# Kernel optimization log

Measured on AMD Instinct MI355X. Metric: run time of the kernel, lower is better.

The kernel has to match this reference:

```python
import jax, jax.numpy as jnp
import numpy as np

SHRINK_THRES = 0.0025
EPS = 1e-12  # F.normalize default eps


def _l2norm(v, axis=-1):
    return v / jnp.maximum(jnp.linalg.norm(v, axis=axis, keepdims=True), EPS)


def setup_inputs() -> dict:
    key = jax.random.key(0)
    ks = jax.random.split(key, 5)
    N, C, H, W = 16, 256, 64, 64
    mem_dim = 512
    x = jax.random.normal(ks[0], (N, C, H, W), dtype=jnp.float32)
    memory = jax.random.normal(ks[1], (mem_dim, C), dtype=jnp.float32) * 0.1
    memory = _l2norm(memory, axis=1)
    w1 = jax.random.normal(ks[2], (C, C // 2), dtype=jnp.float32) * (1.0 / np.sqrt(C))
    b1 = jnp.zeros((C // 2,), dtype=jnp.float32)
    w2 = jax.random.normal(ks[3], (C // 2, C), dtype=jnp.float32) * (1.0 / np.sqrt(C // 2))
    b2 = jnp.zeros((C,), dtype=jnp.float32)
    return {"x": x, "memory": memory, "w1": w1, "b1": b1, "w2": w2, "b2": b2}


def reference(x, memory, w1, b1, w2, b2):
    N, C, H, W = x.shape
    # [N,C,H,W] -> [N*H*W, C]
    x_flat = jnp.transpose(x, (0, 2, 3, 1)).reshape(-1, C)
    x_norm = _l2norm(x_flat, axis=1)
    # shared MLP over memory slots: Linear -> ReLU -> Linear -> ReLU
    m = jax.nn.relu(memory @ w1 + b1)
    m = jax.nn.relu(m @ w2 + b2)
    mem_norm = _l2norm(m, axis=1)  # [M, C]
    # cosine similarity + softmax over memory slots
    att = jax.nn.softmax(x_norm @ mem_norm.T, axis=1)  # [N*H*W, M]
    # hard shrink + L1 renormalization
    att = jax.nn.relu(att - SHRINK_THRES)
    att = att / jnp.maximum(jnp.sum(att, axis=1, keepdims=True), EPS)
    out_flat = att @ mem_norm  # [N*H*W, C]
    output = jnp.transpose(out_flat.reshape(N, H, W, C), (0, 3, 1, 2))
    att_map = jnp.transpose(att.reshape(N, H, W, -1), (0, 3, 1, 2))
    return output, att_map
```

## Files before the change

kernel.cpp:

```cpp
#include <hip/hip_runtime.h>

typedef _Float16 half8 __attribute__((ext_vector_type(8)));
typedef _Float16 half4v __attribute__((ext_vector_type(4)));
typedef float floatx4 __attribute__((ext_vector_type(4)));

#define C_DIM 256
#define M_DIM 512
#define HW 4096
#define TAU 0.0025f
#define LCAP 16

#define BAR_LGKM()                                          \
  do {                                                      \
    asm volatile("s_waitcnt lgkmcnt(0)" ::: "memory");      \
    __builtin_amdgcn_s_barrier();                           \
    __builtin_amdgcn_sched_barrier(0);                      \
  } while (0)

__global__ __launch_bounds__(256) void zero_kernel(float* __restrict__ base)
{
  const floatx4 z = {0.f, 0.f, 0.f, 0.f};
  floatx4* p = (floatx4*)base + (size_t)blockIdx.x * 256 + threadIdx.x;
#pragma unroll
  for (int k = 0; k < 16; ++k)
    __builtin_nontemporal_store(z, p + (size_t)k * 786432);
}

__global__ __launch_bounds__(128) void prep_kernel(
    const float* __restrict__ memory, const float* __restrict__ w1,
    const float* __restrict__ b1, const float* __restrict__ w2,
    const float* __restrict__ b2,
    _Float16* __restrict__ mN, float* __restrict__ mN32)
{
  __shared__ float sm[256];
  __shared__ float sh[128];
  __shared__ float s_part[2];
  __shared__ float s_tot;
  const int r = blockIdx.x;
  const int t = threadIdx.x;

  sm[t]       = memory[r * C_DIM + t];
  sm[t + 128] = memory[r * C_DIM + t + 128];
  __syncthreads();
  float acc = b1[t];
#pragma unroll 8
  for (int c = 0; c < 256; ++c) acc = fmaf(sm[c], w1[c * 128 + t], acc);
  sh[t] = fmaxf(acc, 0.f);
  __syncthreads();
  float o0 = b2[t], o1 = b2[t + 128];
#pragma unroll 8
  for (int k = 0; k < 128; ++k) {
    float h = sh[k];
    o0 = fmaf(h, w2[k * 256 + t], o0);
    o1 = fmaf(h, w2[k * 256 + t + 128], o1);
  }
  o0 = fmaxf(o0, 0.f);
  o1 = fmaxf(o1, 0.f);
  float ss = o0 * o0 + o1 * o1;
#pragma unroll
  for (int off = 32; off >= 1; off >>= 1) ss += __shfl_down(ss, off);
  if ((t & 63) == 0) s_part[t >> 6] = ss;
  __syncthreads();
  if (t == 0) s_tot = s_part[0] + s_part[1];
  __syncthreads();
  const float inv = 1.f / fmaxf(sqrtf(s_tot), 1e-12f);
  const float v0 = o0 * inv, v1 = o1 * inv;
  mN[r * C_DIM + t]        = (_Float16)v0;
  mN[r * C_DIM + t + 128]  = (_Float16)v1;
  mN32[r * C_DIM + t]       = v0;
  mN32[r * C_DIM + t + 128] = v1;
}

#define MFMA16(a, b, c) __builtin_amdgcn_mfma_f32_16x16x32_f16(a, b, c, 0, 0, 0)

__global__ __launch_bounds__(512, 6) void main_kernel(
    const float* __restrict__ x,
    const _Float16* __restrict__ mN,
    const float* __restrict__ mN32,
    float* __restrict__ out, float* __restrict__ attmap)
{
  __shared__ _Float16       Xh[32][264];
  __shared__ unsigned short s_lslot[32][LCAP];
  __shared__ float          s_lval[32][LCAP];
  __shared__ int      s_cnt[32];
  __shared__ float    s_sumsq[32];
  __shared__ float    s_sum1[32];
  __shared__ float    s_sum2[32];

  const int tid  = threadIdx.x;
  const int wave = tid >> 6;
  const int lane = tid & 63;
  const int q    = lane >> 4;
  const int c16  = lane & 15;
  const int g    = tid >> 3;
  const int pxq  = tid & 7;

  const int blk = blockIdx.x;
  const int img = blk >> 7;
  const int hw0 = (blk & 127) * 32;
  const float* __restrict__ xb = x + (size_t)img * C_DIM * HW + hw0;

  if (tid < 32) {
    s_sumsq[tid] = 0.f; s_sum1[tid] = 0.f; s_sum2[tid] = 0.f; s_cnt[tid] = 0;
  }
  __syncthreads();

  {
    floatx4 v[4];
#pragma unroll
    for (int i = 0; i < 4; ++i)
      v[i] = *(const floatx4*)(xb + (size_t)(4 * g + i) * HW + pxq * 4);
    float ps[4];
#pragma unroll
    for (int j = 0; j < 4; ++j) {
      const int p = pxq * 4 + j;
      half4v hv = {(_Float16)v[0][j], (_Float16)v[1][j], (_Float16)v[2][j], (_Float16)v[3][j]};
      *(half4v*)&Xh[p][4 * g] = hv;
      ps[j] = v[0][j] * v[0][j] + v[1][j] * v[1][j] + v[2][j] * v[2][j] + v[3][j] * v[3][j];
    }
#pragma unroll
    for (int off = 8; off < 64; off <<= 1)
#pragma unroll
      for (int j = 0; j < 4; ++j) ps[j] += __shfl_xor(ps[j], off);
    if ((lane >> 3) == 0) {
#pragma unroll
      for (int j = 0; j < 4; ++j) atomicAdd(&s_sumsq[4 * (lane & 7) + j], ps[j]);
    }
  }

  const _Float16* bp[4];
#pragma unroll
  for (int nt = 0; nt < 4; ++nt)
    bp[nt] = mN + (size_t)(wave * 64 + nt * 16 + c16) * C_DIM + q * 8;

  __syncthreads();

  floatx4 acc[2][4];
#pragma unroll
  for (int mt = 0; mt < 2; ++mt)
#pragma unroll
    for (int nt = 0; nt < 4; ++nt) {
      floatx4 z = {0.f, 0.f, 0.f, 0.f};
      acc[mt][nt] = z;
    }
#pragma unroll
  for (int kb = 0; kb < 8; ++kb) {
    half8 bv[4];
#pragma unroll
    for (int nt = 0; nt < 4; ++nt) bv[nt] = *(const half8*)(bp[nt] + kb * 32);
    const int k0 = kb * 32 + q * 8;
    half8 a0 = *(const half8*)&Xh[c16][k0];
    half8 a1 = *(const half8*)&Xh[16 + c16][k0];
#pragma unroll
    for (int nt = 0; nt < 4; ++nt) {
      acc[0][nt] = MFMA16(a0, bv[nt], acc[0][nt]);
      acc[1][nt] = MFMA16(a1, bv[nt], acc[1][nt]);
    }
  }

#pragma unroll
  for (int mt = 0; mt < 2; ++mt)
#pragma unroll
    for (int r = 0; r < 4; ++r) {
      const int m = mt * 16 + q * 4 + r;
      const float iv = 1.f / fmaxf(sqrtf(s_sumsq[m]), 1e-12f);
      float s = 0.f;
#pragma unroll
      for (int nt = 0; nt < 4; ++nt) {
        const float e = __expf(acc[mt][nt][r] * iv);
        acc[mt][nt][r] = e;
        s += e;
      }
      s += __shfl_xor(s, 1);
      s += __shfl_xor(s, 2);
      s += __shfl_xor(s, 4);
      s += __shfl_xor(s, 8);
      if (c16 == 0) atomicAdd(&s_sum1[m], s);
    }
  __syncthreads();

#pragma unroll
  for (int mt = 0; mt < 2; ++mt)
#pragma unroll
    for (int r = 0; r < 4; ++r) {
      const int m = mt * 16 + q * 4 + r;
      const float isum = 1.f / s_sum1[m];
      float s = 0.f;
#pragma unroll
      for (int nt = 0; nt < 4; ++nt) {
        const float tv = fmaxf(acc[mt][nt][r] * isum - TAU, 0.f);
        acc[mt][nt][r] = tv;
        s += tv;
      }
      s += __shfl_xor(s, 1);
      s += __shfl_xor(s, 2);
      s += __shfl_xor(s, 4);
      s += __shfl_xor(s, 8);
      if (c16 == 0) atomicAdd(&s_sum2[m], s);
    }
  __syncthreads();

#pragma unroll
  for (int mt = 0; mt < 2; ++mt) {
    float rs[4];
#pragma unroll
    for (int r = 0; r < 4; ++r)
      rs[r] = 1.f / fmaxf(s_sum2[mt * 16 + q * 4 + r], 1e-12f);
#pragma unroll
    for (int nt = 0; nt < 4; ++nt) {
      floatx4 a4 = acc[mt][nt];
      const unsigned n = wave * 64 + nt * 16 + c16;
#pragma unroll
      for (int r = 0; r < 4; ++r) {
        a4[r] *= rs[r];
        if (a4[r] > 0.f) {
          const int m = mt * 16 + q * 4 + r;
          const int idx = atomicAdd(&s_cnt[m], 1);
          if (idx < LCAP) {
            s_lslot[m][idx] = (unsigned short)n;
            s_lval[m][idx]  = a4[r];
          }
          attmap[((size_t)img * M_DIM + n) * HW + hw0 + m] = a4[r];
        }
      }
    }
  }
  BAR_LGKM();

  const int px4 = (tid & 7) * 4;
  const int chg = tid >> 3;
  int cn[4];
  int any = 0;
#pragma unroll
  for (int p = 0; p < 4; ++p) { cn[p] = min(s_cnt[px4 + p], LCAP); any += cn[p]; }
  if (any) {
    floatx4 f[4] = {{0.f,0.f,0.f,0.f},{0.f,0.f,0.f,0.f},{0.f,0.f,0.f,0.f},{0.f,0.f,0.f,0.f}};
#pragma unroll
    for (int p = 0; p < 4; ++p) {
      for (int j = 0; j < cn[p]; ++j) {
        const int slot  = s_lslot[px4 + p][j];
        const float v   = s_lval[px4 + p][j];
        const floatx4 r0 = *(const floatx4*)(mN32 + (size_t)slot * C_DIM + chg * 4);
        f[0][p] += v * r0[0]; f[1][p] += v * r0[1];
        f[2][p] += v * r0[2]; f[3][p] += v * r0[3];
      }
    }
#pragma unroll
    for (int c = 0; c < 4; ++c)
      *(floatx4*)(out + ((size_t)img * C_DIM + chg * 4 + c) * HW + hw0 + px4) = f[c];
  }
}

extern "C" void kernel_launch(void* const* d_in, const int* in_sizes, int n_in,
                              void* d_out, int out_size, void* d_ws, size_t ws_size,
                              hipStream_t stream) {
  (void)in_sizes; (void)n_in; (void)out_size; (void)ws_size;
  const float* x      = (const float*)d_in[0];
  const float* memory = (const float*)d_in[1];
  const float* w1     = (const float*)d_in[2];
  const float* b1     = (const float*)d_in[3];
  const float* w2     = (const float*)d_in[4];
  const float* b2     = (const float*)d_in[5];
  float* out    = (float*)d_out;
  float* attmap = out + (size_t)16 * C_DIM * HW;

  _Float16* mN   = (_Float16*)d_ws;
  float*    mN32 = (float*)((char*)d_ws + (size_t)M_DIM * C_DIM * sizeof(_Float16));

  hipLaunchKernelGGL(zero_kernel, dim3(3072), dim3(256), 0, stream, out);
  hipLaunchKernelGGL(prep_kernel, dim3(M_DIM), dim3(128), 0, stream,
                     memory, w1, b1, w2, b2, mN, mN32);
  hipLaunchKernelGGL(main_kernel, dim3(2048), dim3(512), 0, stream,
                     x, mN, mN32, out, attmap);
}
```

Before: 351.3 us.

## Halve pixels per block to double grid size and raise occupancy

New measurement: 389.2 us. 1.11x slower.

```diff
diff --git a/kernel.cpp b/kernel.cpp
--- a/kernel.cpp
+++ b/kernel.cpp
@@ -3,6 +3,7 @@
 typedef _Float16 half8 __attribute__((ext_vector_type(8)));
 typedef _Float16 half4v __attribute__((ext_vector_type(4)));
 typedef float floatx4 __attribute__((ext_vector_type(4)));
+typedef float floatx2 __attribute__((ext_vector_type(2)));
 
 #define C_DIM 256
 #define M_DIM 512
@@ -73,39 +74,39 @@
 
 #define MFMA16(a, b, c) __builtin_amdgcn_mfma_f32_16x16x32_f16(a, b, c, 0, 0, 0)
 
-__global__ __launch_bounds__(512, 6) void main_kernel(
+__global__ __launch_bounds__(512, 8) void main_kernel(
     const float* __restrict__ x,
     const _Float16* __restrict__ mN,
     const float* __restrict__ mN32,
     float* __restrict__ out, float* __restrict__ attmap)
 {
-  __shared__ _Float16       Xh[32][264];
-  __shared__ unsigned short s_lslot[32][LCAP];
-  __shared__ float          s_lval[32][LCAP];
-  __shared__ int      s_cnt[32];
-  __shared__ float    s_sumsq[32];
-  __shared__ float    s_sum1[32];
-  __shared__ float    s_sum2[32];
+  __shared__ _Float16       Xh[16][264];
+  __shared__ unsigned short s_lslot[16][LCAP];
+  __shared__ float          s_lval[16][LCAP];
+  __shared__ int      s_cnt[16];
+  __shared__ float    s_sumsq[16];
+  __shared__ float    s_sum1[16];
+  __shared__ float    s_sum2[16];
 
   const int tid  = threadIdx.x;
   const int wave = tid >> 6;
   const int lane = tid & 63;
   const int q    = lane >> 4;
   const int c16  = lane & 15;
-  const int g    = tid >> 3;
-  const int pxq  = tid & 7;
 
   const int blk = blockIdx.x;
-  const int img = blk >> 7;
-  const int hw0 = (blk & 127) * 32;
+  const int img = blk >> 8;
+  const int hw0 = (blk & 255) * 16;
   const float* __restrict__ xb = x + (size_t)img * C_DIM * HW + hw0;
 
-  if (tid < 32) {
+  if (tid < 16) {
     s_sumsq[tid] = 0.f; s_sum1[tid] = 0.f; s_sum2[tid] = 0.f; s_cnt[tid] = 0;
   }
   __syncthreads();
 
-  {
+  if (tid < 256) {
+    const int g   = tid >> 2;
+    const int pxq = tid & 3;
     floatx4 v[4];
 #pragma unroll
     for (int i = 0; i < 4; ++i)
@@ -119,12 +120,12 @@
       ps[j] = v[0][j] * v[0][j] + v[1][j] * v[1][j] + v[2][j] * v[2][j] + v[3][j] * v[3][j];
     }
 #pragma unroll
-    for (int off = 8; off < 64; off <<= 1)
+    for (int off = 4; off < 64; off <<= 1)
 #pragma unroll
       for (int j = 0; j < 4; ++j) ps[j] += __shfl_xor(ps[j], off);
-    if ((lane >> 3) == 0) {
-#pragma unroll
-      for (int j = 0; j < 4; ++j) atomicAdd(&s_sumsq[4 * (lane & 7) + j], ps[j]);
+    if (lane < 4) {
+#pragma unroll
+      for (int j = 0; j < 4; ++j) atomicAdd(&s_sumsq[lane * 4 + j], ps[j]);
     }
   }
 
@@ -135,14 +136,12 @@
 
   __syncthreads();
 
-  floatx4 acc[2][4];
-#pragma unroll
-  for (int mt = 0; mt < 2; ++mt)
-#pragma unroll
-    for (int nt = 0; nt < 4; ++nt) {
-      floatx4 z = {0.f, 0.f, 0.f, 0.f};
-      acc[mt][nt] = z;
-    }
+  floatx4 acc[4];
+#pragma unroll
+  for (int nt = 0; nt < 4; ++nt) {
+    floatx4 z = {0.f, 0.f, 0.f, 0.f};
+    acc[nt] = z;
+  }
 #pragma unroll
   for (int kb = 0; kb < 8; ++kb) {
     half8 bv[4];
@@ -150,71 +149,62 @@
     for (int nt = 0; nt < 4; ++nt) bv[nt] = *(const half8*)(bp[nt] + kb * 32);
     const int k0 = kb * 32 + q * 8;
     half8 a0 = *(const half8*)&Xh[c16][k0];
-    half8 a1 = *(const half8*)&Xh[16 + c16][k0];
+#pragma unroll
+    for (int nt = 0; nt < 4; ++nt) acc[nt] = MFMA16(a0, bv[nt], acc[nt]);
+  }
+
+#pragma unroll
+  for (int r = 0; r < 4; ++r) {
+    const int m = q * 4 + r;
+    const float iv = 1.f / fmaxf(sqrtf(s_sumsq[m]), 1e-12f);
+    float s = 0.f;
 #pragma unroll
     for (int nt = 0; nt < 4; ++nt) {
-      acc[0][nt] = MFMA16(a0, bv[nt], acc[0][nt]);
-      acc[1][nt] = MFMA16(a1, bv[nt], acc[1][nt]);
-    }
-  }
-
-#pragma unroll
-  for (int mt = 0; mt < 2; ++mt)
-#pragma unroll
-    for (int r = 0; r < 4; ++r) {
-      const int m = mt * 16 + q * 4 + r;
-      const float iv = 1.f / fmaxf(sqrtf(s_sumsq[m]), 1e-12f);
-      float s = 0.f;
-#pragma unroll
-      for (int nt = 0; nt < 4; ++nt) {
-        const float e = __expf(acc[mt][nt][r] * iv);
-        acc[mt][nt][r] = e;
-        s += e;
-      }
-      s += __shfl_xor(s, 1);
-      s += __shfl_xor(s, 2);
-      s += __shfl_xor(s, 4);
-      s += __shfl_xor(s, 8);
-      if (c16 == 0) atomicAdd(&s_sum1[m], s);
-    }
-  __syncthreads();
-
-#pragma unroll
-  for (int mt = 0; mt < 2; ++mt)
-#pragma unroll
-    for (int r = 0; r < 4; ++r) {
-      const int m = mt * 16 + q * 4 + r;
-      const float isum = 1.f / s_sum1[m];
-      float s = 0.f;
-#pragma unroll
-      for (int nt = 0; nt < 4; ++nt) {
-        const float tv = fmaxf(acc[mt][nt][r] * isum - TAU, 0.f);
-        acc[mt][nt][r] = tv;
-        s += tv;
-      }
-      s += __shfl_xor(s, 1);
-      s += __shfl_xor(s, 2);
-      s += __shfl_xor(s, 4);
-      s += __shfl_xor(s, 8);
-      if (c16 == 0) atomicAdd(&s_sum2[m], s);
-    }
-  __syncthreads();
-
-#pragma unroll
-  for (int mt = 0; mt < 2; ++mt) {
+      const float e = __expf(acc[nt][r] * iv);
+      acc[nt][r] = e;
+      s += e;
+    }
+    s += __shfl_xor(s, 1);
+    s += __shfl_xor(s, 2);
+    s += __shfl_xor(s, 4);
+    s += __shfl_xor(s, 8);
+    if (c16 == 0) atomicAdd(&s_sum1[m], s);
+  }
+  __syncthreads();
+
+#pragma unroll
+  for (int r = 0; r < 4; ++r) {
+    const int m = q * 4 + r;
+    const float isum = 1.f / s_sum1[m];
+    float s = 0.f;
+#pragma unroll
+    for (int nt = 0; nt < 4; ++nt) {
+      const float tv = fmaxf(acc[nt][r] * isum - TAU, 0.f);
+      acc[nt][r] = tv;
+      s += tv;
+    }
+    s += __shfl_xor(s, 1);
+    s += __shfl_xor(s, 2);
+    s += __shfl_xor(s, 4);
+    s += __shfl_xor(s, 8);
+    if (c16 == 0) atomicAdd(&s_sum2[m], s);
+  }
+  __syncthreads();
+
+  {
     float rs[4];
 #pragma unroll
     for (int r = 0; r < 4; ++r)
-      rs[r] = 1.f / fmaxf(s_sum2[mt * 16 + q * 4 + r], 1e-12f);
+      rs[r] = 1.f / fmaxf(s_sum2[q * 4 + r], 1e-12f);
 #pragma unroll
     for (int nt = 0; nt < 4; ++nt) {
-      floatx4 a4 = acc[mt][nt];
+      floatx4 a4 = acc[nt];
       const unsigned n = wave * 64 + nt * 16 + c16;
 #pragma unroll
       for (int r = 0; r < 4; ++r) {
         a4[r] *= rs[r];
         if (a4[r] > 0.f) {
-          const int m = mt * 16 + q * 4 + r;
+          const int m = q * 4 + r;
           const int idx = atomicAdd(&s_cnt[m], 1);
           if (idx < LCAP) {
             s_lslot[m][idx] = (unsigned short)n;
@@ -227,27 +217,27 @@
   }
   BAR_LGKM();
 
-  const int px4 = (tid & 7) * 4;
-  const int chg = tid >> 3;
+  const int px4 = (tid & 3) * 4;
+  const int chp = tid >> 2;
   int cn[4];
   int any = 0;
 #pragma unroll
   for (int p = 0; p < 4; ++p) { cn[p] = min(s_cnt[px4 + p], LCAP); any += cn[p]; }
   if (any) {
-    floatx4 f[4] = {{0.f,0.f,0.f,0.f},{0.f,0.f,0.f,0.f},{0.f,0.f,0.f,0.f},{0.f,0.f,0.f,0.f}};
+    floatx4 f[2] = {{0.f,0.f,0.f,0.f},{0.f,0.f,0.f,0.f}};
 #pragma unroll
     for (int p = 0; p < 4; ++p) {
       for (int j = 0; j < cn[p]; ++j) {
         const int slot  = s_lslot[px4 + p][j];
         const float v   = s_lval[px4 + p][j];
-        const floatx4 r0 = *(const floatx4*)(mN32 + (size_t)slot * C_DIM + chg * 4);
-        f[0][p] += v * r0[0]; f[1][p] += v * r0[1];
-        f[2][p] += v * r0[2]; f[3][p] += v * r0[3];
+        const floatx2 r01 = *(const floatx2*)(mN32 + (size_t)slot * C_DIM + 2 * chp);
+        f[0][p] += v * r01[0];
+        f[1][p] += v * r01[1];
       }
     }
 #pragma unroll
-    for (int c = 0; c < 4; ++c)
-      *(floatx4*)(out + ((size_t)img * C_DIM + chg * 4 + c) * HW + hw0 + px4) = f[c];
+    for (int c = 0; c < 2; ++c)
+      *(floatx4*)(out + ((size_t)img * C_DIM + 2 * chp + c) * HW + hw0 + px4) = f[c];
   }
 }
 
@@ -270,6 +260,6 @@
   hipLaunchKernelGGL(zero_kernel, dim3(3072), dim3(256), 0, stream, out);
   hipLaunchKernelGGL(prep_kernel, dim3(M_DIM), dim3(128), 0, stream,
                      memory, w1, b1, w2, b2, mN, mN32);
-  hipLaunchKernelGGL(main_kernel, dim3(2048), dim3(512), 0, stream,
+  hipLaunchKernelGGL(main_kernel, dim3(4096), dim3(512), 0, stream,
                      x, mN, mN32, out, attmap);
 }
```
